# Optimization experiments

Measured on AMD Instinct MI355X. Metric: run time of the kernel, lower is better.

Reference implementation:

```python
import jax, jax.numpy as jnp
import numpy as np

CHUNK = 512          # size_FHT
K = 28               # size_k (Hadamard-28)
HIDDEN = CHUNK * K   # 14336 = actual_input_size
SCALE = 1.0 / np.sqrt(np.float32(HIDDEN))

_H28_ROWS = [
    "++++++++++++++-+++++++++++++",
    "+++-++----++-++-+-++----++-+",
    "++++-++----++-++-+-++----++-",
    "+-+++-++----+++-+-+-++----++",
    "++-+++-++----+++-+-+-++----+",
    "+++-+++-++----+++-+-+-++----",
    "+-++-+++-++---+-++-+-+-++---",
    "+--++-+++-++--+--++-+-+-++--",
    "+---++-+++-++-+---++-+-+-++-",
    "+----++-+++-+++----++-+-+-++",
    "++----++-+++-+++----++-+-+-+",
    "+++----++-+++-+++----++-+-+-",
    "+-++----++-++++-++----++-+-+",
    "++-++----++-++++-++----++-+-",
    "-+++++++++++++--------------",
    "+-+-++----++-+---+--++++--+-",
    "++-+-++----++-----+--++++--+",
    "+-+-+-++----++-+---+--++++--",
    "++-+-+-++----+--+---+--++++-",
    "+++-+-+-++-------+---+--++++",
    "+-++-+-+-++----+--+---+--+++",
    "+--++-+-+-++---++--+---+--++",
    "+---++-+-+-++--+++--+---+--+",
    "+----++-+-+-++-++++--+---+--",
    "++----++-+-+-+--++++--+---+-",
    "+++----++-+-+----++++--+---+",
    "+-++----++-+-+-+--++++--+---",
    "++-++----++-+---+--++++--+--",
]

def _make_h28():
    m = np.array([[1.0 if c == '+' else -1.0 for c in row] for row in _H28_ROWS],
                 dtype=np.float32)
    return jnp.asarray(m)  # [28, 28]


def fwht(x):
    """Fast Walsh-Hadamard transform over last dim (power of 2), O(n log n)."""
    n = x.shape[-1]
    orig_shape = x.shape
    x = x.reshape(-1, n)
    h = 1
    while h < n:
        x = x.reshape(-1, n // (2 * h), 2, h)
        a, b = x[:, :, 0, :], x[:, :, 1, :]
        x = jnp.stack([a + b, a - b], axis=2).reshape(-1, n)
        h *= 2
    return x.reshape(orig_shape)


def setup_inputs() -> dict:
    key = jax.random.key(0)
    k1, _ = jax.random.split(key)
    X = jax.random.normal(k1, (4096, HIDDEN), dtype=jnp.float32)
    H28 = _make_h28()
    return {"X": X, "H28": H28}


def reference(X, H28):
    og_shape = X.shape
    # 1) per-512-chunk fast Hadamard transform, scaled by 1/sqrt(14336)
    Xc = X.reshape(-1, CHUNK)          # [T*K, 512]
    Xc = fwht(Xc) * jnp.asarray(SCALE, X.dtype)
    # 2) left-multiply by H28 across the k=28 chunk groups
    Xk = Xc.reshape(-1, K, CHUNK)      # [T, 28, 512]
    Y = jnp.einsum('ij,tjc->tic', H28.astype(X.dtype), Xk)
    return Y.reshape(og_shape)
```

## Files before the change

### kernel.cpp

```cpp
#include <hip/hip_runtime.h>

#define HIDDEN 14336

constexpr char HS[28][29] = {
    "++++++++++++++-+++++++++++++",
    "+++-++----++-++-+-++----++-+",
    "++++-++----++-++-+-++----++-",
    "+-+++-++----+++-+-+-++----++",
    "++-+++-++----+++-+-+-++----+",
    "+++-+++-++----+++-+-+-++----",
    "+-++-+++-++---+-++-+-+-++---",
    "+--++-+++-++--+--++-+-+-++--",
    "+---++-+++-++-+---++-+-+-++-",
    "+----++-+++-+++----++-+-+-++",
    "++----++-+++-+++----++-+-+-+",
    "+++----++-+++-+++----++-+-+-",
    "+-++----++-++++-++----++-+-+",
    "++-++----++-++++-++----++-+-",
    "-+++++++++++++--------------",
    "+-+-++----++-+---+--++++--+-",
    "++-+-++----++-----+--++++--+",
    "+-+-+-++----++-+---+--++++--",
    "++-+-+-++----+--+---+--++++-",
    "+++-+-+-++-------+---+--++++",
    "+-++-+-+-++----+--+---+--+++",
    "+--++-+-+-++---++--+---+--++",
    "+---++-+-+-++--+++--+---+--+",
    "+----++-+-+-++-++++--+---+--",
    "++----++-+-+-+--++++--+---+-",
    "+++----++-+-+----++++--+---+",
    "+-++----++-+-+-+--++++--+---",
    "++-++----++-+---+--++++--+--",
};

static __device__ __forceinline__ void fwht16(float (&v)[16]) {
    #pragma unroll
    for (int h = 1; h < 16; h <<= 1) {
        #pragma unroll
        for (int i = 0; i < 16; ++i) {
            if ((i & h) == 0) {
                const float a = v[i], b = v[i | h];
                v[i] = a + b;
                v[i | h] = a - b;
            }
        }
    }
}

template <int CTRL>
static __device__ __forceinline__ float bfly_dpp(float x, int sm) {
    const int fi = __float_as_int(x);
    const int p = __builtin_amdgcn_update_dpp(fi, fi, CTRL, 0xF, 0xF, false);
    return __int_as_float(p) + __int_as_float(fi ^ sm);
}

template <int PAT>
static __device__ __forceinline__ float bfly_swz(float x, int sm) {
    const int fi = __float_as_int(x);
    const int p = __builtin_amdgcn_ds_swizzle(fi, PAT);
    return __int_as_float(p) + __int_as_float(fi ^ sm);
}

static __device__ __forceinline__ void fwht_cross32(float (&v)[16], int sm1, int sm2,
                                                    int sm4, int sm8, int sm16) {
    #pragma unroll
    for (int k = 0; k < 16; ++k) v[k] = bfly_dpp<0xB1>(v[k], sm1);
    #pragma unroll
    for (int k = 0; k < 16; ++k) v[k] = bfly_dpp<0x4E>(v[k], sm2);
    #pragma unroll
    for (int k = 0; k < 16; ++k) v[k] = bfly_swz<0x101F>(v[k], sm4);
    #pragma unroll
    for (int k = 0; k < 16; ++k) v[k] = bfly_swz<0x201F>(v[k], sm8);
    #pragma unroll
    for (int k = 0; k < 16; ++k) v[k] = bfly_swz<0x401F>(v[k], sm16);
}

__global__ __launch_bounds__(448) void quarot_kernel(const float* __restrict__ X,
                                                     float* __restrict__ Y) {
    __shared__ float s[HIDDEN];
    const int tid = threadIdx.x;
    const int l = tid & 63;
    const int w = tid >> 6;
    const int q = l & 31;
    const int h = l >> 5;
    const int sm1 = (q & 1) ? 0x80000000 : 0;
    const int sm2 = (q & 2) ? 0x80000000 : 0;
    const int sm4 = (q & 4) ? 0x80000000 : 0;
    const int sm8 = (q & 8) ? 0x80000000 : 0;
    const int sm16 = (q & 16) ? 0x80000000 : 0;

    const float* __restrict__ xr = X + (size_t)blockIdx.x * HIDDEN;
    float* __restrict__ yr = Y + (size_t)blockIdx.x * HIDDEN;
    const float scale = 1.0f / sqrtf((float)HIDDEN);

    const int cA = 4 * w + h;
    const int cB = 4 * w + 2 + h;

    float vA[16], vB[16];
    {
        const float* pA = xr + cA * 512 + q * 16;
        const float* pB = xr + cB * 512 + q * 16;
        #pragma unroll
        for (int g = 0; g < 4; ++g) {
            const float4 a = *reinterpret_cast<const float4*>(pA + 4 * g);
            vA[4 * g + 0] = a.x * scale; vA[4 * g + 1] = a.y * scale;
            vA[4 * g + 2] = a.z * scale; vA[4 * g + 3] = a.w * scale;
        }
        #pragma unroll
        for (int g = 0; g < 4; ++g) {
            const float4 b = *reinterpret_cast<const float4*>(pB + 4 * g);
            vB[4 * g + 0] = b.x * scale; vB[4 * g + 1] = b.y * scale;
            vB[4 * g + 2] = b.z * scale; vB[4 * g + 3] = b.w * scale;
        }
    }

    fwht16(vA);
    fwht_cross32(vA, sm1, sm2, sm4, sm8, sm16);
    {
        const int r = q >> 2;
        #pragma unroll
        for (int g = 0; g < 4; ++g) {
            const int slot = ((4 * q + g) & 15) ^ r;
            *reinterpret_cast<float4*>(s + cA * 512 + r * 64 + 4 * slot) =
                make_float4(vA[4 * g + 0], vA[4 * g + 1], vA[4 * g + 2], vA[4 * g + 3]);
        }
    }

    fwht16(vB);
    fwht_cross32(vB, sm1, sm2, sm4, sm8, sm16);
    {
        const int r = q >> 2;
        #pragma unroll
        for (int g = 0; g < 4; ++g) {
            const int slot = ((4 * q + g) & 15) ^ r;
            *reinterpret_cast<float4*>(s + cB * 512 + r * 64 + 4 * slot) =
                make_float4(vB[4 * g + 0], vB[4 * g + 1], vB[4 * g + 2], vB[4 * g + 3]);
        }
    }

    __syncthreads();

    for (int c = tid; c < 512; c += 448) {
        const int rr = c >> 6;
        const int boff = rr * 64 + 4 * (((c >> 2) & 15) ^ rr) + (c & 3);
        float u[14], d[14];
        #pragma unroll
        for (int j = 0; j < 14; ++j) {
            const float a = s[j * 512 + boff];
            const float b = s[(j + 14) * 512 + boff];
            u[j] = a + b;
            d[j] = a - b;
        }
        const float Su = (((u[0] + u[1]) + (u[2] + u[3])) + ((u[4] + u[5]) + (u[6] + u[7]))) +
                         (((u[8] + u[9]) + (u[10] + u[11])) + (u[12] + u[13]));
        const float Sd = (((d[0] + d[1]) + (d[2] + d[3])) + ((d[4] + d[5]) + (d[6] + d[7]))) +
                         (((d[8] + d[9]) + (d[10] + d[11])) + (d[12] + d[13]));
        #pragma unroll
        for (int i = 0; i < 14; ++i) {
            float nu = 0.0f, nd = 0.0f;
            #pragma unroll
            for (int j = 0; j < 14; ++j) {
                if (j != i && HS[i][j] == '-') {
                    nu += u[j];
                    nd += d[j];
                }
            }
            const float Cu = fmaf(-2.0f, nu, Su - u[i]);
            const float Cd = fmaf(-2.0f, nd, Sd - d[i]);
            yr[i * 512 + c] = Cu + d[i];
            yr[(i + 14) * 512 + c] = Cd - u[i];
        }
    }
}

extern "C" void kernel_launch(void* const* d_in, const int* in_sizes, int n_in,
                              void* d_out, int out_size, void* d_ws, size_t ws_size,
                              hipStream_t stream) {
    const float* X = (const float*)d_in[0];
    float* Y = (float*)d_out;
    const int rows = in_sizes[0] / HIDDEN;
    quarot_kernel<<<dim3(rows), dim3(448), 0, stream>>>(X, Y);
}
```

Baseline: 91.35 us.

## Process eight rows per persistent block with prefetch of next row's input

Each block now handles eight consecutive rows in a loop instead of one row per block. The global loads for the next row are issued before the H28 mixing phase of the current row, so memory latency overlaps with LDS reads and the output stores. It also adds a launch-bounds occupancy hint and replaces __syncthreads with raw barriers. The cost is fewer blocks (512 instead of 4096) and a grid that assumes the row count divides by eight.

```diff
diff --git a/kernel.cpp b/kernel.cpp
--- a/kernel.cpp
+++ b/kernel.cpp
@@ -1,6 +1,7 @@
 #include <hip/hip_runtime.h>
 
 #define HIDDEN 14336
+#define NROWS_PER_BLOCK 8
 
 constexpr char HS[28][29] = {
     "++++++++++++++-+++++++++++++",
@@ -75,8 +76,48 @@
     for (int k = 0; k < 16; ++k) v[k] = bfly_swz<0x401F>(v[k], sm16);
 }
 
-__global__ __launch_bounds__(448) void quarot_kernel(const float* __restrict__ X,
-                                                     float* __restrict__ Y) {
+static __device__ __forceinline__ void load16(const float* __restrict__ p, float (&v)[16]) {
+    #pragma unroll
+    for (int g = 0; g < 4; ++g) {
+        const float4 t = *reinterpret_cast<const float4*>(p + 4 * g);
+        v[4 * g + 0] = t.x; v[4 * g + 1] = t.y;
+        v[4 * g + 2] = t.z; v[4 * g + 3] = t.w;
+    }
+}
+
+static __device__ __forceinline__ void mix_col(const float* __restrict__ s, int boff,
+                                               float* __restrict__ yr, int c) {
+    float u[14], d[14];
+    #pragma unroll
+    for (int j = 0; j < 14; ++j) {
+        const float a = s[j * 512 + boff];
+        const float b = s[(j + 14) * 512 + boff];
+        u[j] = a + b;
+        d[j] = a - b;
+    }
+    const float Su = (((u[0] + u[1]) + (u[2] + u[3])) + ((u[4] + u[5]) + (u[6] + u[7]))) +
+                     (((u[8] + u[9]) + (u[10] + u[11])) + (u[12] + u[13]));
+    const float Sd = (((d[0] + d[1]) + (d[2] + d[3])) + ((d[4] + d[5]) + (d[6] + d[7]))) +
+                     (((d[8] + d[9]) + (d[10] + d[11])) + (d[12] + d[13]));
+    #pragma unroll
+    for (int i = 0; i < 14; ++i) {
+        float nu = 0.0f, nd = 0.0f;
+        #pragma unroll
+        for (int j = 0; j < 14; ++j) {
+            if (j != i && HS[i][j] == '-') {
+                nu += u[j];
+                nd += d[j];
+            }
+        }
+        const float Cu = fmaf(-2.0f, nu, Su - u[i]);
+        const float Cd = fmaf(-2.0f, nd, Sd - d[i]);
+        yr[i * 512 + c] = Cu + d[i];
+        yr[(i + 14) * 512 + c] = Cd - u[i];
+    }
+}
+
+__global__ __launch_bounds__(448, 4) void quarot_kernel(const float* __restrict__ X,
+                                                        float* __restrict__ Y) {
     __shared__ float s[HIDDEN];
     const int tid = threadIdx.x;
     const int l = tid & 63;
@@ -89,87 +130,64 @@
     const int sm8 = (q & 8) ? 0x80000000 : 0;
     const int sm16 = (q & 16) ? 0x80000000 : 0;
 
-    const float* __restrict__ xr = X + (size_t)blockIdx.x * HIDDEN;
-    float* __restrict__ yr = Y + (size_t)blockIdx.x * HIDDEN;
-    const float scale = 1.0f / sqrtf((float)HIDDEN);
-
     const int cA = 4 * w + h;
     const int cB = 4 * w + 2 + h;
+    const int offA = cA * 512 + q * 16;
+    const int offB = cB * 512 + q * 16;
+    const int rq = q >> 2;
+
+    const int c0 = tid;
+    const int rr0 = c0 >> 6;
+    const int boff0 = rr0 * 64 + 4 * (((c0 >> 2) & 15) ^ rr0) + (c0 & 3);
+    const int c1 = tid + 448;
+    const int boff1 = 7 * 64 + 4 * (((c1 >> 2) & 15) ^ 7) + (c1 & 3);
+
+    const size_t row0 = (size_t)blockIdx.x * NROWS_PER_BLOCK;
+    const float* __restrict__ xr = X + row0 * (size_t)HIDDEN;
+    float* __restrict__ yb = Y + row0 * (size_t)HIDDEN;
+    const float scale = 1.0f / sqrtf((float)HIDDEN);
 
     float vA[16], vB[16];
-    {
-        const float* pA = xr + cA * 512 + q * 16;
-        const float* pB = xr + cB * 512 + q * 16;
+    load16(xr + offA, vA);
+    load16(xr + offB, vB);
+
+    #pragma unroll 1
+    for (int r = 0; r < NROWS_PER_BLOCK; ++r) {
+        #pragma unroll
+        for (int k = 0; k < 16; ++k) { vA[k] *= scale; vB[k] *= scale; }
+        fwht16(vA);
+        fwht_cross32(vA, sm1, sm2, sm4, sm8, sm16);
+        fwht16(vB);
+        fwht_cross32(vB, sm1, sm2, sm4, sm8, sm16);
+
+        asm volatile("s_waitcnt lgkmcnt(0)" ::: "memory");
+        __builtin_amdgcn_s_barrier();
+
         #pragma unroll
         for (int g = 0; g < 4; ++g) {
-            const float4 a = *reinterpret_cast<const float4*>(pA + 4 * g);
-            vA[4 * g + 0] = a.x * scale; vA[4 * g + 1] = a.y * scale;
-            vA[4 * g + 2] = a.z * scale; vA[4 * g + 3] = a.w * scale;
+            const int slot = ((4 * q + g) & 15) ^ rq;
+            *reinterpret_cast<float4*>(s + cA * 512 + rq * 64 + 4 * slot) =
+                make_float4(vA[4 * g + 0], vA[4 * g + 1], vA[4 * g + 2], vA[4 * g + 3]);
         }
         #pragma unroll
         for (int g = 0; g < 4; ++g) {
-            const float4 b = *reinterpret_cast<const float4*>(pB + 4 * g);
-            vB[4 * g + 0] = b.x * scale; vB[4 * g + 1] = b.y * scale;
-            vB[4 * g + 2] = b.z * scale; vB[4 * g + 3] = b.w * scale;
-        }
-    }
-
-    fwht16(vA);
-    fwht_cross32(vA, sm1, sm2, sm4, sm8, sm16);
-    {
-        const int r = q >> 2;
-        #pragma unroll
-        for (int g = 0; g < 4; ++g) {
-            const int slot = ((4 * q + g) & 15) ^ r;
-            *reinterpret_cast<float4*>(s + cA * 512 + r * 64 + 4 * slot) =
-                make_float4(vA[4 * g + 0], vA[4 * g + 1], vA[4 * g + 2], vA[4 * g + 3]);
-        }
-    }
-
-    fwht16(vB);
-    fwht_cross32(vB, sm1, sm2, sm4, sm8, sm16);
-    {
-        const int r = q >> 2;
-        #pragma unroll
-        for (int g = 0; g < 4; ++g) {
-            const int slot = ((4 * q + g) & 15) ^ r;
-            *reinterpret_cast<float4*>(s + cB * 512 + r * 64 + 4 * slot) =
+            const int slot = ((4 * q + g) & 15) ^ rq;
+            *reinterpret_cast<float4*>(s + cB * 512 + rq * 64 + 4 * slot) =
                 make_float4(vB[4 * g + 0], vB[4 * g + 1], vB[4 * g + 2], vB[4 * g + 3]);
         }
-    }
-
-    __syncthreads();
-
-    for (int c = tid; c < 512; c += 448) {
-        const int rr = c >> 6;
-        const int boff = rr * 64 + 4 * (((c >> 2) & 15) ^ rr) + (c & 3);
-        float u[14], d[14];
-        #pragma unroll
-        for (int j = 0; j < 14; ++j) {
-            const float a = s[j * 512 + boff];
-            const float b = s[(j + 14) * 512 + boff];
-            u[j] = a + b;
-            d[j] = a - b;
-        }
-        const float Su = (((u[0] + u[1]) + (u[2] + u[3])) + ((u[4] + u[5]) + (u[6] + u[7]))) +
-                         (((u[8] + u[9]) + (u[10] + u[11])) + (u[12] + u[13]));
-        const float Sd = (((d[0] + d[1]) + (d[2] + d[3])) + ((d[4] + d[5]) + (d[6] + d[7]))) +
-                         (((d[8] + d[9]) + (d[10] + d[11])) + (d[12] + d[13]));
-        #pragma unroll
-        for (int i = 0; i < 14; ++i) {
-            float nu = 0.0f, nd = 0.0f;
-            #pragma unroll
-            for (int j = 0; j < 14; ++j) {
-                if (j != i && HS[i][j] == '-') {
-                    nu += u[j];
-                    nd += d[j];
-                }
-            }
-            const float Cu = fmaf(-2.0f, nu, Su - u[i]);
-            const float Cd = fmaf(-2.0f, nd, Sd - d[i]);
-            yr[i * 512 + c] = Cu + d[i];
-            yr[(i + 14) * 512 + c] = Cd - u[i];
-        }
+
+        if (r + 1 < NROWS_PER_BLOCK) {
+            const float* xn = xr + (size_t)(r + 1) * HIDDEN;
+            load16(xn + offA, vA);
+            load16(xn + offB, vB);
+        }
+
+        asm volatile("s_waitcnt lgkmcnt(0)" ::: "memory");
+        __builtin_amdgcn_s_barrier();
+
+        float* __restrict__ yr = yb + (size_t)r * HIDDEN;
+        mix_col(s, boff0, yr, c0);
+        if (tid < 64) mix_col(s, boff1, yr, c1);
     }
 }
 
@@ -179,5 +197,6 @@
     const float* X = (const float*)d_in[0];
     float* Y = (float*)d_out;
     const int rows = in_sizes[0] / HIDDEN;
-    quarot_kernel<<<dim3(rows), dim3(448), 0, stream>>>(X, Y);
-}
+    const int nblk = rows / NROWS_PER_BLOCK;
+    quarot_kernel<<<dim3(nblk), dim3(448), 0, stream>>>(X, Y);
+}
```

Result: slower. 112.3 us (+22.9%).
